# Optimization experiments

Hardware: AMD Instinct MI355X
Metric: run time of the kernel (lower is better)

## Reference

```python
import jax, jax.numpy as jnp
import numpy as np

N = 100000
IN_C, HID, OUT_D, NUM_CLASSES = 256, 64, 64, 6
E = 1600000


def setup_inputs() -> dict:
    key = jax.random.key(0)
    ks = jax.random.split(key, 12)
    glorot = lambda k, fi, fo: jax.random.normal(k, (fi, fo), jnp.float32) * np.sqrt(2.0 / (fi + fo))
    return {
        "x": jax.random.normal(ks[0], (N, IN_C), jnp.float32),
        "edge_index": jax.random.randint(ks[1], (2, E), 0, N, jnp.int64),
        "W1": glorot(ks[2], IN_C, HID), "b1": jnp.zeros((HID,), jnp.float32),
        "W2": glorot(ks[3], HID, HID), "b2": jnp.zeros((HID,), jnp.float32),
        "Wp": glorot(ks[4], HID, OUT_D), "bp": jnp.zeros((OUT_D,), jnp.float32),
        "Wc": glorot(ks[5], OUT_D, NUM_CLASSES), "bc": jnp.zeros((NUM_CLASSES,), jnp.float32),
    }


def _gcn_norm(edge_index, n):
    # add self-loops, symmetric normalization D^{-1/2}(A+I)D^{-1/2} (PyG gcn_norm)
    loop = jnp.arange(n, dtype=edge_index.dtype)
    src = jnp.concatenate([edge_index[0], loop])
    dst = jnp.concatenate([edge_index[1], loop])
    deg = jax.ops.segment_sum(jnp.ones_like(dst, jnp.float32), dst, num_segments=n)
    dinv = jnp.where(deg > 0, jax.lax.rsqrt(deg), 0.0)
    norm = dinv[src] * dinv[dst]  # [E+N]
    return src, dst, norm


def _gcn_conv(x, W, b, src, dst, norm, n):
    h = x @ W  # dense GEMM first (PyG order)
    msg = h[src] * norm[:, None]  # gather + scale over edges
    out = jax.ops.segment_sum(msg, dst, num_segments=n)  # scatter-add aggregate
    return out + b


def reference(x, edge_index, W1, b1, W2, b2, Wp, bp, Wc, bc):
    n = x.shape[0]
    src, dst, norm = _gcn_norm(edge_index, n)
    h = jax.nn.relu(_gcn_conv(x, W1, b1, src, dst, norm, n))
    # dropout is inactive in eval mode (training=False)
    h = jax.nn.relu(_gcn_conv(h, W2, b2, src, dst, norm, n))
    z = jax.nn.relu(h @ Wp + bp)
    logits = z @ Wc + bc
    return (logits, z)
```

## Files before the change

### kernel.cpp

```cpp
#include <hip/hip_runtime.h>

#define N_NODES 100000
#define IN_CH   256
#define HID_D   64
#define NCLS    6
#define NE      1600000
#define WB      64
#define OVF_CAP 4096
#define NPART   8
#define PSZ     (N_NODES / NPART)

typedef unsigned short u16;
typedef unsigned int   u32;
typedef __attribute__((ext_vector_type(8))) short bf16x8;
typedef __attribute__((ext_vector_type(4))) float f32x4;
typedef __attribute__((ext_vector_type(2))) int   i32x2;

#define OFF_CNT   0u
#define OFF_OVFC  400000u
#define OFF_OVF   400128u
#define OFF_COL   433152u
#define OFF_G     26033152u
#define OFF_H     38833152u
#define Z_OFF     600000u

__device__ __forceinline__ u16 f2bf(float f) {
    u32 u = __float_as_uint(f);
    return (u16)((u + 0x7fffu + ((u >> 16) & 1u)) >> 16);
}
__device__ __forceinline__ float bf2f(u16 h) {
    return __uint_as_float(((u32)h) << 16);
}

__global__ __launch_bounds__(256) void k_fill(const int* __restrict__ ei,
                                              int* __restrict__ cnt,
                                              int* __restrict__ col,
                                              int* __restrict__ ovfc,
                                              int* __restrict__ ovf) {
    const int part = blockIdx.x & (NPART - 1);
    const int lo = part * PSZ;
    const int hi = lo + PSZ;
    const int e0 = (blockIdx.x >> 3) * 512 + threadIdx.x * 2;
    i32x2 s2 = __builtin_nontemporal_load((const i32x2*)(ei + e0));
    i32x2 d2 = __builtin_nontemporal_load((const i32x2*)(ei + NE + e0));
#pragma unroll
    for (int j = 0; j < 2; ++j) {
        int s = s2[j];
        int d = d2[j];
        if (d < lo || d >= hi) continue;
        if ((u32)s >= (u32)N_NODES) continue;
        int p = atomicAdd(&cnt[d], 1);
        if (p < WB) {
            col[(size_t)d * WB + p] = s;
        } else {
            int k = atomicAdd(ovfc, 1);
            if (k < OVF_CAP) { ovf[2 * k] = s; ovf[2 * k + 1] = d; }
        }
    }
}

template <int KDIM, bool ABF16>
__global__ __launch_bounds__(256) void k_gemm(const void* __restrict__ A,
                                              const float* __restrict__ W,
                                              const int* __restrict__ cnt,
                                              u16* __restrict__ G) {
    constexpr int KK = KDIM / 32;
    __shared__ __align__(16) u16 sB[KK * 4 * 64 * 8];

    for (int idx = threadIdx.x; idx < KK * 2048; idx += 256) {
        int j = idx & 7, l = (idx >> 3) & 63, t = (idx >> 9) & 3, kk = idx >> 11;
        int k = kk * 32 + (l >> 4) * 8 + j;
        int c = t * 16 + (l & 15);
        sB[idx] = f2bf(W[k * 64 + c]);
    }
    __syncthreads();

    const int lane = threadIdx.x & 63;
    const int wv   = threadIdx.x >> 6;
    const int row0 = blockIdx.x * 64 + wv * 16;
    const int g4   = lane >> 4;
    const int r16  = lane & 15;

    int arow = row0 + r16;
    int arow_c = arow < N_NODES ? arow : 0;

    f32x4 acc[4] = {{0,0,0,0},{0,0,0,0},{0,0,0,0},{0,0,0,0}};

    for (int kk = 0; kk < KK; ++kk) {
        bf16x8 a;
        if (ABF16) {
            const u16* ap = (const u16*)A + (size_t)arow_c * KDIM + kk * 32 + g4 * 8;
            a = *(const bf16x8*)ap;
        } else {
            const float* ap = (const float*)A + (size_t)arow_c * KDIM + kk * 32 + g4 * 8;
            float4 f0 = *(const float4*)ap;
            float4 f1 = *(const float4*)(ap + 4);
            a[0] = (short)f2bf(f0.x); a[1] = (short)f2bf(f0.y);
            a[2] = (short)f2bf(f0.z); a[3] = (short)f2bf(f0.w);
            a[4] = (short)f2bf(f1.x); a[5] = (short)f2bf(f1.y);
            a[6] = (short)f2bf(f1.z); a[7] = (short)f2bf(f1.w);
        }
#pragma unroll
        for (int t = 0; t < 4; ++t) {
            bf16x8 b = *(const bf16x8*)&sB[((kk * 4 + t) * 64 + lane) * 8];
            acc[t] = __builtin_amdgcn_mfma_f32_16x16x32_bf16(a, b, acc[t], 0, 0, 0);
        }
    }

#pragma unroll
    for (int r = 0; r < 4; ++r) {
        int row = row0 + g4 * 4 + r;
        if (row < N_NODES) {
            float dinv = rsqrtf((float)(cnt[row] + 1));
#pragma unroll
            for (int t = 0; t < 4; ++t)
                G[(size_t)row * 64 + t * 16 + r16] = f2bf(acc[t][r] * dinv);
        }
    }
}

__global__ __launch_bounds__(256) void k_agg(const u16* __restrict__ G,
                                             const int* __restrict__ col,
                                             const int* __restrict__ cnt,
                                             const int* __restrict__ ovfc,
                                             const int* __restrict__ ovf,
                                             const float* __restrict__ bias,
                                             u16* __restrict__ Hout) {
    int node = blockIdx.x * 4 + (threadIdx.x >> 6);
    int lane = threadIdx.x & 63;

    int deg = cnt[node];
    int m = min(deg, WB);
    int mycol = col[(size_t)node * WB + lane];

    float acc = bf2f(G[(size_t)node * 64 + lane]);

    int e = 0;
    for (; e + 4 <= m; e += 4) {
        int c0 = __shfl(mycol, e + 0), c1 = __shfl(mycol, e + 1);
        int c2 = __shfl(mycol, e + 2), c3 = __shfl(mycol, e + 3);
        float v0 = bf2f(G[(size_t)c0 * 64 + lane]);
        float v1 = bf2f(G[(size_t)c1 * 64 + lane]);
        float v2 = bf2f(G[(size_t)c2 * 64 + lane]);
        float v3 = bf2f(G[(size_t)c3 * 64 + lane]);
        acc += v0; acc += v1; acc += v2; acc += v3;
    }
    for (; e < m; ++e) {
        int c = __shfl(mycol, e);
        acc += bf2f(G[(size_t)c * 64 + lane]);
    }

    int no = *ovfc;
    if (no > 0) {
        no = min(no, OVF_CAP);
        for (int j = 0; j < no; ++j)
            if (ovf[2 * j + 1] == node)
                acc += bf2f(G[(size_t)ovf[2 * j] * 64 + lane]);
    }

    float dinv = rsqrtf((float)(deg + 1));
    float v = fmaxf(acc * dinv + bias[lane], 0.f);
    Hout[(size_t)node * 64 + lane] = f2bf(v);
}

__global__ __launch_bounds__(256) void k_mlp(const u16* __restrict__ H,
                                             const float* __restrict__ Wp,
                                             const float* __restrict__ bp,
                                             const float* __restrict__ Wc,
                                             const float* __restrict__ bc,
                                             float* __restrict__ out) {
    __shared__ __align__(16) u16 sP[2 * 4 * 64 * 8];
    __shared__ __align__(16) u16 sC[2 * 64 * 8];
    __shared__ __align__(16) u16 zt[4][16][72];

    for (int idx = threadIdx.x; idx < 4096; idx += 256) {
        int j = idx & 7, l = (idx >> 3) & 63, t = (idx >> 9) & 3, kk = idx >> 11;
        int k = kk * 32 + (l >> 4) * 8 + j;
        int c = t * 16 + (l & 15);
        sP[idx] = f2bf(Wp[k * 64 + c]);
    }
    for (int idx = threadIdx.x; idx < 1024; idx += 256) {
        int j = idx & 7, l = (idx >> 3) & 63, kk = idx >> 9;
        int k = kk * 32 + (l >> 4) * 8 + j;
        int c = l & 15;
        sC[idx] = (c < NCLS) ? f2bf(Wc[k * NCLS + c]) : (u16)0;
    }
    __syncthreads();

    const int lane = threadIdx.x & 63;
    const int wv   = threadIdx.x >> 6;
    const int row0 = blockIdx.x * 64 + wv * 16;
    const int g4   = lane >> 4;
    const int r16  = lane & 15;

    int arow = row0 + r16;
    int arow_c = arow < N_NODES ? arow : (N_NODES - 1);

    f32x4 zac[4] = {{0,0,0,0},{0,0,0,0},{0,0,0,0},{0,0,0,0}};
#pragma unroll
    for (int kk = 0; kk < 2; ++kk) {
        bf16x8 a = *(const bf16x8*)((const u16*)H + (size_t)arow_c * 64 + kk * 32 + g4 * 8);
#pragma unroll
        for (int t = 0; t < 4; ++t) {
            bf16x8 b = *(const bf16x8*)&sP[((kk * 4 + t) * 64 + lane) * 8];
            zac[t] = __builtin_amdgcn_mfma_f32_16x16x32_bf16(a, b, zac[t], 0, 0, 0);
        }
    }

#pragma unroll
    for (int r = 0; r < 4; ++r) {
        int row = row0 + g4 * 4 + r;
#pragma unroll
        for (int t = 0; t < 4; ++t) {
            float v = zac[t][r] + bp[t * 16 + r16];
            v = fmaxf(v, 0.f);
            zt[wv][g4 * 4 + r][t * 16 + r16] = f2bf(v);
            if (row < N_NODES)
                out[(size_t)Z_OFF + (size_t)row * 64 + t * 16 + r16] = v;
        }
    }
    __syncthreads();

    f32x4 lac = {0, 0, 0, 0};
#pragma unroll
    for (int kk = 0; kk < 2; ++kk) {
        bf16x8 a = *(const bf16x8*)&zt[wv][r16][kk * 32 + g4 * 8];
        bf16x8 b = *(const bf16x8*)&sC[(kk * 64 + lane) * 8];
        lac = __builtin_amdgcn_mfma_f32_16x16x32_bf16(a, b, lac, 0, 0, 0);
    }
#pragma unroll
    for (int r = 0; r < 4; ++r) {
        int row = row0 + g4 * 4 + r;
        if (row < N_NODES && r16 < NCLS)
            out[(size_t)row * NCLS + r16] = lac[r] + bc[r16];
    }
}

extern "C" void kernel_launch(void* const* d_in, const int* in_sizes, int n_in,
                              void* d_out, int out_size, void* d_ws, size_t ws_size,
                              hipStream_t stream) {
    const float* x  = (const float*)d_in[0];
    const int*   ei = (const int*)d_in[1];
    const float* W1 = (const float*)d_in[2];
    const float* b1 = (const float*)d_in[3];
    const float* W2 = (const float*)d_in[4];
    const float* b2 = (const float*)d_in[5];
    const float* Wp = (const float*)d_in[6];
    const float* bp = (const float*)d_in[7];
    const float* Wc = (const float*)d_in[8];
    const float* bc = (const float*)d_in[9];
    float* out = (float*)d_out;

    char* ws  = (char*)d_ws;
    int* cnt  = (int*)(ws + OFF_CNT);
    int* ovfc = (int*)(ws + OFF_OVFC);
    int* ovf  = (int*)(ws + OFF_OVF);
    int* col  = (int*)(ws + OFF_COL);
    u16* g    = (u16*)(ws + OFF_G);
    u16* h    = (u16*)(ws + OFF_H);

    const int GB = (N_NODES + 63) / 64;

    (void)hipMemsetAsync(ws, 0, OFF_OVF, stream);
    k_fill<<<(NE / 512) * NPART, 256, 0, stream>>>(ei, cnt, col, ovfc, ovf);
    k_gemm<IN_CH, false><<<GB, 256, 0, stream>>>(x, W1, cnt, g);
    k_agg<<<N_NODES / 4, 256, 0, stream>>>(g, col, cnt, ovfc, ovf, b1, h);
    k_gemm<HID_D, true><<<GB, 256, 0, stream>>>(h, W2, cnt, g);
    k_agg<<<N_NODES / 4, 256, 0, stream>>>(g, col, cnt, ovfc, ovf, b2, h);
    k_mlp<<<GB, 256, 0, stream>>>(h, Wp, bp, Wc, bc, out);
}
```

Measured before the change: 249.5 us.

## Bucket edges by destination partition before CSR fill

Replaces the fill kernel, which launched once per partition and re-read the whole edge list eight times, with a two-pass scheme. A partition kernel stages edges per destination partition in shared memory and appends them to per-partition global queues. A second kernel then fills the adjacency lists from each queue, so the atomics still go to a localized destination range without eight full edge reads. It adds an extra kernel launch and a queue buffer that aliases the G region, with a fixed per-partition capacity that silently drops edges on overflow.

```diff
diff --git a/kernel.cpp b/kernel.cpp
--- a/kernel.cpp
+++ b/kernel.cpp
@@ -9,6 +9,7 @@
 #define OVF_CAP 4096
 #define NPART   8
 #define PSZ     (N_NODES / NPART)
+#define QCAP    204800
 
 typedef unsigned short u16;
 typedef unsigned int   u32;
@@ -18,10 +19,12 @@
 
 #define OFF_CNT   0u
 #define OFF_OVFC  400000u
+#define OFF_QCNT  400032u
 #define OFF_OVF   400128u
 #define OFF_COL   433152u
 #define OFF_G     26033152u
 #define OFF_H     38833152u
+#define OFF_QBUF  OFF_G
 #define Z_OFF     600000u
 
 __device__ __forceinline__ u16 f2bf(float f) {
@@ -32,23 +35,62 @@
     return __uint_as_float(((u32)h) << 16);
 }
 
-__global__ __launch_bounds__(256) void k_fill(const int* __restrict__ ei,
-                                              int* __restrict__ cnt,
-                                              int* __restrict__ col,
-                                              int* __restrict__ ovfc,
-                                              int* __restrict__ ovf) {
-    const int part = blockIdx.x & (NPART - 1);
-    const int lo = part * PSZ;
-    const int hi = lo + PSZ;
-    const int e0 = (blockIdx.x >> 3) * 512 + threadIdx.x * 2;
+__global__ __launch_bounds__(256) void k_part(const int* __restrict__ ei,
+                                              int* __restrict__ qcnt,
+                                              int2* __restrict__ qbuf) {
+    __shared__ int2 stage[NPART][128];
+    __shared__ int lcnt[NPART], cc[NPART], gb[NPART];
+    const int tid = threadIdx.x;
+    if (tid < NPART) lcnt[tid] = 0;
+    __syncthreads();
+
+    const int e0 = blockIdx.x * 512 + tid * 2;
     i32x2 s2 = __builtin_nontemporal_load((const i32x2*)(ei + e0));
     i32x2 d2 = __builtin_nontemporal_load((const i32x2*)(ei + NE + e0));
+
+    int pp[2], pos[2];
 #pragma unroll
     for (int j = 0; j < 2; ++j) {
-        int s = s2[j];
         int d = d2[j];
-        if (d < lo || d >= hi) continue;
-        if ((u32)s >= (u32)N_NODES) continue;
+        int p = (u32)d < (u32)N_NODES ? d / PSZ : 0;
+        pp[j] = p;
+        pos[j] = atomicAdd(&lcnt[p], 1);
+        if (pos[j] < 128) stage[p][pos[j]] = make_int2(s2[j], d);
+    }
+    __syncthreads();
+    if (tid < NPART) {
+        cc[tid] = min(lcnt[tid], 128);
+        gb[tid] = atomicAdd(&qcnt[tid], cc[tid]);
+    }
+    __syncthreads();
+    for (int i = tid; i < NPART * 128; i += 256) {
+        int q = i >> 7, idx = i & 127;
+        if (idx < cc[q] && gb[q] + idx < QCAP)
+            qbuf[q * QCAP + gb[q] + idx] = stage[q][idx];
+    }
+#pragma unroll
+    for (int j = 0; j < 2; ++j) {
+        if (pos[j] >= 128) {
+            int k = atomicAdd(&qcnt[pp[j]], 1);
+            if (k < QCAP) qbuf[pp[j] * QCAP + k] = make_int2(s2[j], d2[j]);
+        }
+    }
+}
+
+__global__ __launch_bounds__(256) void k_fill2(const int2* __restrict__ qbuf,
+                                               const int* __restrict__ qcnt,
+                                               int* __restrict__ cnt,
+                                               int* __restrict__ col,
+                                               int* __restrict__ ovfc,
+                                               int* __restrict__ ovf) {
+    const int part = blockIdx.x & (NPART - 1);
+    const int n = min(qcnt[part], QCAP);
+    const int2* q = qbuf + (size_t)part * QCAP;
+    const int stride = (gridDim.x >> 3) * 256;
+    for (int i = (blockIdx.x >> 3) * 256 + threadIdx.x; i < n; i += stride) {
+        int2 e = q[i];
+        int s = e.x, d = e.y;
+        if ((u32)s >= (u32)N_NODES || (u32)d >= (u32)N_NODES) continue;
         int p = atomicAdd(&cnt[d], 1);
         if (p < WB) {
             col[(size_t)d * WB + p] = s;
@@ -251,18 +293,21 @@
     const float* bc = (const float*)d_in[9];
     float* out = (float*)d_out;
 
-    char* ws  = (char*)d_ws;
-    int* cnt  = (int*)(ws + OFF_CNT);
-    int* ovfc = (int*)(ws + OFF_OVFC);
-    int* ovf  = (int*)(ws + OFF_OVF);
-    int* col  = (int*)(ws + OFF_COL);
-    u16* g    = (u16*)(ws + OFF_G);
-    u16* h    = (u16*)(ws + OFF_H);
+    char* ws   = (char*)d_ws;
+    int*  cnt  = (int*)(ws + OFF_CNT);
+    int*  ovfc = (int*)(ws + OFF_OVFC);
+    int*  qcnt = (int*)(ws + OFF_QCNT);
+    int*  ovf  = (int*)(ws + OFF_OVF);
+    int*  col  = (int*)(ws + OFF_COL);
+    int2* qbuf = (int2*)(ws + OFF_QBUF);
+    u16*  g    = (u16*)(ws + OFF_G);
+    u16*  h    = (u16*)(ws + OFF_H);
 
     const int GB = (N_NODES + 63) / 64;
 
     (void)hipMemsetAsync(ws, 0, OFF_OVF, stream);
-    k_fill<<<(NE / 512) * NPART, 256, 0, stream>>>(ei, cnt, col, ovfc, ovf);
+    k_part<<<NE / 512, 256, 0, stream>>>(ei, qcnt, qbuf);
+    k_fill2<<<128 * NPART, 256, 0, stream>>>(qbuf, qcnt, cnt, col, ovfc, ovf);
     k_gemm<IN_CH, false><<<GB, 256, 0, stream>>>(x, W1, cnt, g);
     k_agg<<<N_NODES / 4, 256, 0, stream>>>(g, col, cnt, ovfc, ovf, b1, h);
     k_gemm<HID_D, true><<<GB, 256, 0, stream>>>(h, W2, cnt, g);
```

New measurement: 284.9 us. +14.2%, slower.
